# Kernel tuning notes

Hardware: AMD Instinct MI355X
Metric: run time of the kernel (lower is better)

The kernel has to match this reference:

```python
import jax, jax.numpy as jnp
import numpy as np

NUM_EXPERTS_TOTAL = 9  # 8 routed + 1 shared (shared expert is also routed via softmax in this module)
TOP_K = 2


def setup_inputs() -> dict:
    key = jax.random.key(0)
    k0, k1, k2, k3, k4 = jax.random.split(key, 5)
    B, S, H, I = 2, 2048, 1024, 2816
    E = NUM_EXPERTS_TOTAL
    x = jax.random.normal(k0, (B, S, H), dtype=jnp.float32)
    Wr = (jax.random.normal(k1, (H, E), dtype=jnp.float32) * 0.02)          # router (no bias)
    Wg = (jax.random.normal(k2, (E, H, I), dtype=jnp.float32) * 0.02)       # gate_proj per expert
    Wu = (jax.random.normal(k3, (E, H, I), dtype=jnp.float32) * 0.02)       # up_proj per expert
    Wd = (jax.random.normal(k4, (E, I, H), dtype=jnp.float32) * 0.02)       # down_proj per expert
    return {"x": x, "Wr": Wr, "Wg": Wg, "Wu": Wu, "Wd": Wd}


def reference(x, Wr, Wg, Wu, Wd):
    B, S, H = x.shape
    E = NUM_EXPERTS_TOTAL
    T = B * S

    # Router: softmax over all 9 experts, then top-2 and renormalize
    logits = jnp.einsum('bsh,he->bse', x, Wr)
    probs = jax.nn.softmax(logits, axis=-1)
    topk_w, topk_idx = jax.lax.top_k(probs, TOP_K)                 # [B,S,K]
    topk_w = topk_w / jnp.sum(topk_w, axis=-1, keepdims=True)

    xf = x.reshape(T, H)
    wf = topk_w.reshape(T, TOP_K)
    idxf = topk_idx.reshape(T, TOP_K)

    # Per-token combine weight for each expert (0 if not selected)
    cw = jnp.zeros((T, E), dtype=x.dtype).at[jnp.arange(T)[:, None], idxf].add(wf)  # [T,E]

    # SwiGLU MLP for every expert (tokens with cw==0 contribute nothing)
    gate = jax.nn.silu(jnp.einsum('th,ehi->tei', xf, Wg))          # [T,E,I]
    hidden = gate * jnp.einsum('th,ehi->tei', xf, Wu)              # [T,E,I]
    out = jnp.einsum('tei,eih,te->th', hidden, Wd, cw)             # weighted combine
    return out.reshape(B, S, H)
```

## Files before the change

### kernel.cpp

```cpp
#include <hip/hip_runtime.h>
#include <cstdint>
#include <cstddef>

#define T_TOK 4096
#define H_DIM 1024
#define I_DIM 2816
#define E_NUM 9
#define MAXTILE 76

typedef __bf16 bf16;
typedef bf16 bf16x4 __attribute__((ext_vector_type(4)));
typedef bf16 bf16x8 __attribute__((ext_vector_type(8)));
typedef float f32x4 __attribute__((ext_vector_type(4)));

constexpr int BM = 128, BN = 128, BK = 32;
constexpr int HTILE = BM * BK;
constexpr size_t HI = (size_t)H_DIM * I_DIM;

constexpr int XCAST_BLKS  = T_TOK * H_DIM / 2048;
constexpr int TGU_BLKS    = (I_DIM / 64) * (H_DIM / 64) * 2 * E_NUM;
constexpr int ROUTER_BLKS = T_TOK / 4;
constexpr int PRE1_BLKS   = XCAST_BLKS + TGU_BLKS + ROUTER_BLKS;

constexpr int GU_BLKS = (I_DIM / BN) * MAXTILE;
constexpr int TD_BLKS = (H_DIM / 64) * (I_DIM / 64) * E_NUM;
constexpr int MAIN1_BLKS = GU_BLKS + TD_BLKS;

#define GL16(gp, lp)                                                                   \
  __builtin_amdgcn_global_load_lds((const __attribute__((address_space(1))) void*)(gp), \
                                   (__attribute__((address_space(3))) void*)(lp), 16, 0, 0)

__device__ __forceinline__ void transpose_tile(float* __restrict__ tile,
                                               const float* __restrict__ src,
                                               bf16* __restrict__ dst, int R, int C,
                                               int bx, int by) {
  int r0 = by * 64, c0 = bx * 64;
  int t = threadIdx.x;
#pragma unroll
  for (int h = 0; h < 4; ++h) {
    int idx = h * 256 + t;
    int row = idx >> 4;
    int col = (idx & 15) * 4;
    GL16(src + (size_t)(r0 + row) * C + c0 + col, &tile[idx * 4]);
  }
  __syncthreads();
  int oc = t >> 2;
  int q  = t & 3;
  bf16x8 w0, w1;
#pragma unroll
  for (int j = 0; j < 8; ++j) w0[j] = (bf16)tile[(q * 16 + j) * 64 + oc];
#pragma unroll
  for (int j = 0; j < 8; ++j) w1[j] = (bf16)tile[(q * 16 + 8 + j) * 64 + oc];
  bf16* dp = dst + (size_t)(c0 + oc) * R + r0 + q * 16;
  *reinterpret_cast<bf16x8*>(dp)     = w0;
  *reinterpret_cast<bf16x8*>(dp + 8) = w1;
}

__global__ __launch_bounds__(256) void k_pre1(const float* __restrict__ x,
                                              bf16* __restrict__ xb,
                                              const float* __restrict__ Wg,
                                              const float* __restrict__ Wu,
                                              bf16* __restrict__ WgT,
                                              bf16* __restrict__ WuT,
                                              const float* __restrict__ Wr,
                                              int* __restrict__ ridx,
                                              float* __restrict__ rw,
                                              int* __restrict__ counts) {
  __shared__ float tile[64 * 64];
  int b = blockIdx.x;

  if (b < XCAST_BLKS) {
    size_t i = ((size_t)b * 256 + threadIdx.x) * 8;
    float4 a = *reinterpret_cast<const float4*>(x + i);
    float4 c = *reinterpret_cast<const float4*>(x + i + 4);
    bf16x8 v;
    v[0]=(bf16)a.x; v[1]=(bf16)a.y; v[2]=(bf16)a.z; v[3]=(bf16)a.w;
    v[4]=(bf16)c.x; v[5]=(bf16)c.y; v[6]=(bf16)c.z; v[7]=(bf16)c.w;
    *reinterpret_cast<bf16x8*>(xb + i) = v;
    return;
  }
  b -= XCAST_BLKS;

  if (b < TGU_BLKS) {
    int bx = b % (I_DIM / 64);
    int rest = b / (I_DIM / 64);
    int by = rest % (H_DIM / 64);
    int z  = rest / (H_DIM / 64);
    const float* src = (z < 9) ? (Wg + (size_t)z * HI) : (Wu + (size_t)(z - 9) * HI);
    bf16* dst = (z < 9) ? (WgT + (size_t)z * HI) : (WuT + (size_t)(z - 9) * HI);
    transpose_tile(tile, src, dst, H_DIM, I_DIM, bx, by);
    return;
  }
  b -= TGU_BLKS;

  {
    int lane = threadIdx.x & 63;
    int wid  = threadIdx.x >> 6;
    int t = b * 4 + wid;
    const float* xr = x + (size_t)t * H_DIM;
    float acc[E_NUM];
#pragma unroll
    for (int e = 0; e < E_NUM; ++e) acc[e] = 0.f;
    for (int h = lane; h < H_DIM; h += 64) {
      float xv = xr[h];
      const float* wr = Wr + h * E_NUM;
#pragma unroll
      for (int e = 0; e < E_NUM; ++e) acc[e] += xv * wr[e];
    }
#pragma unroll
    for (int off = 32; off > 0; off >>= 1) {
#pragma unroll
      for (int e = 0; e < E_NUM; ++e) acc[e] += __shfl_xor(acc[e], off);
    }
    if (lane == 0) {
      int i0 = 0;
#pragma unroll
      for (int e = 1; e < E_NUM; ++e) if (acc[e] > acc[i0]) i0 = e;
      int i1 = (i0 == 0) ? 1 : 0;
#pragma unroll
      for (int e = 0; e < E_NUM; ++e) if (e != i0 && acc[e] > acc[i1]) i1 = e;
      float r  = expf(acc[i1] - acc[i0]);
      float w0 = 1.f / (1.f + r);
      float w1 = r / (1.f + r);
      ridx[2 * t]     = i0;
      ridx[2 * t + 1] = i1;
      rw[2 * t]     = w0;
      rw[2 * t + 1] = w1;
      atomicAdd(&counts[i0], 1);
      atomicAdd(&counts[i1], 1);
    }
  }
}

__global__ void k_scan(const int* __restrict__ counts, int* __restrict__ offsets,
                       int* __restrict__ cursor, int* __restrict__ tiles,
                       int* __restrict__ n_tiles) {
  if (threadIdx.x == 0) {
    int s = 0, nt = 0;
    for (int e = 0; e < E_NUM; ++e) {
      offsets[e] = s;
      int c = counts[e];
      for (int pt = 0; pt * BM < c && nt < MAXTILE; ++pt) tiles[nt++] = (e << 16) | pt;
      s += c;
    }
    offsets[E_NUM] = s;
    *n_tiles = nt;
  }
  if (threadIdx.x < E_NUM) cursor[threadIdx.x] = 0;
}

__global__ __launch_bounds__(256) void k_scatter(const int* __restrict__ ridx,
                                                 const int* __restrict__ offsets,
                                                 int* __restrict__ cursor,
                                                 int* __restrict__ perm) {
  int t = blockIdx.x * 256 + threadIdx.x;
  if (t >= T_TOK) return;
#pragma unroll
  for (int k = 0; k < 2; ++k) {
    int e = ridx[2 * t + k];
    int pos = atomicAdd(&cursor[e], 1);
    perm[offsets[e] + pos] = 2 * t + k;
  }
}

__global__ __launch_bounds__(256, 2) void k_main1(const bf16* __restrict__ xb,
                                                  const bf16* __restrict__ WgT,
                                                  const bf16* __restrict__ WuT,
                                                  const int* __restrict__ perm,
                                                  const int* __restrict__ offsets,
                                                  const int* __restrict__ tiles,
                                                  const int* __restrict__ n_tiles,
                                                  bf16* __restrict__ hidden,
                                                  const float* __restrict__ Wd,
                                                  bf16* __restrict__ WdT) {
  __shared__ char smem[6 * HTILE * 2];
  int b = blockIdx.x;

  if (b >= GU_BLKS) {
    b -= GU_BLKS;
    int bx = b % (H_DIM / 64);
    int rest = b / (H_DIM / 64);
    int by = rest % (I_DIM / 64);
    int z  = rest / (I_DIM / 64);
    transpose_tile((float*)smem, Wd + (size_t)z * HI, WdT + (size_t)z * HI,
                   I_DIM, H_DIM, bx, by);
    return;
  }

  int ty = b / (I_DIM / BN);
  int n0 = (b % (I_DIM / BN)) * BN;
  if (ty >= *n_tiles) return;
  int tv = tiles[ty];
  int e = tv >> 16, pt = tv & 0xffff;
  int seg0 = offsets[e], cnt = offsets[e + 1] - seg0;

  bf16* As = (bf16*)smem;
  bf16* Bg = As + 2 * HTILE;
  bf16* Bu = As + 4 * HTILE;

  int tid = threadIdx.x, lane = tid & 63, wid = tid >> 6;
  int wm = wid >> 1, wn = wid & 1, l15 = lane & 15, l16 = lane >> 4;

  int srow1 = tid >> 2, srow2 = 64 + srow1;
  int kc = (tid & 3) * 8;
  int p1 = pt * BM + srow1, p2 = pt * BM + srow2;
  const bf16* a1 = xb + (size_t)(perm[seg0 + (p1 < cnt ? p1 : 0)] >> 1) * H_DIM + kc;
  const bf16* a2 = xb + (size_t)(perm[seg0 + (p2 < cnt ? p2 : 0)] >> 1) * H_DIM + kc;
  const bf16* g1 = WgT + ((size_t)e * I_DIM + n0 + srow1) * H_DIM + kc;
  const bf16* g2 = WgT + ((size_t)e * I_DIM + n0 + srow2) * H_DIM + kc;
  const bf16* u1 = WuT + ((size_t)e * I_DIM + n0 + srow1) * H_DIM + kc;
  const bf16* u2 = WuT + ((size_t)e * I_DIM + n0 + srow2) * H_DIM + kc;
  bf16* lA1 = &As[tid * 8];       bf16* lA2 = &As[2048 + tid * 8];
  bf16* lG1 = &Bg[tid * 8];       bf16* lG2 = &Bg[2048 + tid * 8];
  bf16* lU1 = &Bu[tid * 8];       bf16* lU2 = &Bu[2048 + tid * 8];

  f32x4 accg[4][4], accu[4][4];
#pragma unroll
  for (int m = 0; m < 4; ++m)
#pragma unroll
    for (int n = 0; n < 4; ++n) {
      accg[m][n] = (f32x4){0.f, 0.f, 0.f, 0.f};
      accu[m][n] = (f32x4){0.f, 0.f, 0.f, 0.f};
    }

  for (int k0 = 0; k0 < H_DIM; k0 += 2 * BK) {
    GL16(a1 + k0, lA1);            GL16(a2 + k0, lA2);
    GL16(a1 + k0 + BK, lA1 + HTILE); GL16(a2 + k0 + BK, lA2 + HTILE);
    GL16(g1 + k0, lG1);            GL16(g2 + k0, lG2);
    GL16(g1 + k0 + BK, lG1 + HTILE); GL16(g2 + k0 + BK, lG2 + HTILE);
    GL16(u1 + k0, lU1);            GL16(u2 + k0, lU2);
    GL16(u1 + k0 + BK, lU1 + HTILE); GL16(u2 + k0 + BK, lU2 + HTILE);
    __syncthreads();

#pragma unroll
    for (int kk = 0; kk < 2; ++kk) {
      const bf16* Ab = &As[kk * HTILE];
      const bf16* Gb = &Bg[kk * HTILE];
      const bf16* Ub = &Bu[kk * HTILE];
      bf16x8 af[4], bg[4], bu[4];
#pragma unroll
      for (int m = 0; m < 4; ++m)
        af[m] = *reinterpret_cast<const bf16x8*>(&Ab[(wm * 64 + m * 16 + l15) * BK + l16 * 8]);
#pragma unroll
      for (int n = 0; n < 4; ++n) {
        bg[n] = *reinterpret_cast<const bf16x8*>(&Gb[(wn * 64 + n * 16 + l15) * BK + l16 * 8]);
        bu[n] = *reinterpret_cast<const bf16x8*>(&Ub[(wn * 64 + n * 16 + l15) * BK + l16 * 8]);
      }
#pragma unroll
      for (int m = 0; m < 4; ++m)
#pragma unroll
        for (int n = 0; n < 4; ++n) {
          accg[m][n] = __builtin_amdgcn_mfma_f32_16x16x32_bf16(af[m], bg[n], accg[m][n], 0, 0, 0);
          accu[m][n] = __builtin_amdgcn_mfma_f32_16x16x32_bf16(af[m], bu[n], accu[m][n], 0, 0, 0);
        }
    }
    __syncthreads();
  }

#pragma unroll
  for (int m = 0; m < 4; ++m) {
#pragma unroll
    for (int r = 0; r < 4; ++r) {
      int p_glob = pt * BM + wm * 64 + m * 16 + l16 * 4 + r;
      if (p_glob < cnt) {
        bf16* hrow = hidden + (size_t)(seg0 + p_glob) * I_DIM;
#pragma unroll
        for (int n = 0; n < 4; ++n) {
          int col = n0 + wn * 64 + n * 16 + l15;
          float g = accg[m][n][r];
          float u = accu[m][n][r];
          float h = g / (1.f + __expf(-g)) * u;
          hrow[col] = (bf16)h;
        }
      }
    }
  }
}

__global__ __launch_bounds__(256, 2) void k_down(const bf16* __restrict__ hidden,
                                                 const bf16* __restrict__ WdT,
                                                 const int* __restrict__ perm,
                                                 const int* __restrict__ offsets,
                                                 const int* __restrict__ tiles,
                                                 const int* __restrict__ n_tiles,
                                                 bf16* __restrict__ pair_half) {
  if ((int)blockIdx.y >= *n_tiles) return;
  int tv = tiles[blockIdx.y];
  int e = tv >> 16, pt = tv & 0xffff;
  int seg0 = offsets[e], cnt = offsets[e + 1] - seg0;
  int n0 = blockIdx.x * BN;
  int kz = blockIdx.z * (I_DIM / 2);
  bf16* pout = pair_half + (size_t)blockIdx.z * 2 * T_TOK * H_DIM;

  __shared__ bf16 As[2 * HTILE];
  __shared__ bf16 Bs[2 * HTILE];

  int tid = threadIdx.x, lane = tid & 63, wid = tid >> 6;
  int wm = wid >> 1, wn = wid & 1, l15 = lane & 15, l16 = lane >> 4;

  int srow1 = tid >> 2, srow2 = 64 + srow1;
  int kc = (tid & 3) * 8;
  int p1 = pt * BM + srow1, p2 = pt * BM + srow2;
  const bf16* a1 = hidden + (size_t)(seg0 + (p1 < cnt ? p1 : 0)) * I_DIM + kz + kc;
  const bf16* a2 = hidden + (size_t)(seg0 + (p2 < cnt ? p2 : 0)) * I_DIM + kz + kc;
  const bf16* b1 = WdT + ((size_t)e * H_DIM + n0 + srow1) * I_DIM + kz + kc;
  const bf16* b2 = WdT + ((size_t)e * H_DIM + n0 + srow2) * I_DIM + kz + kc;
  bf16* lA1 = &As[tid * 8];  bf16* lA2 = &As[2048 + tid * 8];
  bf16* lB1 = &Bs[tid * 8];  bf16* lB2 = &Bs[2048 + tid * 8];

  f32x4 acc[4][4];
#pragma unroll
  for (int m = 0; m < 4; ++m)
#pragma unroll
    for (int n = 0; n < 4; ++n) acc[m][n] = (f32x4){0.f, 0.f, 0.f, 0.f};

  for (int k0 = 0; k0 < I_DIM / 2; k0 += 2 * BK) {
    GL16(a1 + k0, lA1);            GL16(a2 + k0, lA2);
    GL16(a1 + k0 + BK, lA1 + HTILE); GL16(a2 + k0 + BK, lA2 + HTILE);
    GL16(b1 + k0, lB1);            GL16(b2 + k0, lB2);
    GL16(b1 + k0 + BK, lB1 + HTILE); GL16(b2 + k0 + BK, lB2 + HTILE);
    __syncthreads();

#pragma unroll
    for (int kk = 0; kk < 2; ++kk) {
      const bf16* Ab = &As[kk * HTILE];
      const bf16* Bb = &Bs[kk * HTILE];
      bf16x8 af[4], bfr[4];
#pragma unroll
      for (int m = 0; m < 4; ++m)
        af[m] = *reinterpret_cast<const bf16x8*>(&Ab[(wm * 64 + m * 16 + l15) * BK + l16 * 8]);
#pragma unroll
      for (int n = 0; n < 4; ++n)
        bfr[n] = *reinterpret_cast<const bf16x8*>(&Bb[(wn * 64 + n * 16 + l15) * BK + l16 * 8]);
#pragma unroll
      for (int m = 0; m < 4; ++m)
#pragma unroll
        for (int n = 0; n < 4; ++n)
          acc[m][n] = __builtin_amdgcn_mfma_f32_16x16x32_bf16(af[m], bfr[n], acc[m][n], 0, 0, 0);
    }
    __syncthreads();
  }

#pragma unroll
  for (int m = 0; m < 4; ++m) {
#pragma unroll
    for (int r = 0; r < 4; ++r) {
      int p_glob = pt * BM + wm * 64 + m * 16 + l16 * 4 + r;
      if (p_glob < cnt) {
        int pair = perm[seg0 + p_glob];
        bf16* orow = pout + (size_t)pair * H_DIM;
#pragma unroll
        for (int n = 0; n < 4; ++n) {
          int col = n0 + wn * 64 + n * 16 + l15;
          orow[col] = (bf16)acc[m][n][r];
        }
      }
    }
  }
}

__global__ __launch_bounds__(256) void k_combine(const bf16* __restrict__ pair_half,
                                                 const float* __restrict__ rw,
                                                 float* __restrict__ out) {
  int t = blockIdx.x;
  int c = threadIdx.x;
  const bf16* z0 = pair_half;
  const bf16* z1 = pair_half + (size_t)2 * T_TOK * H_DIM;
  float w0 = rw[2 * t];
  float w1 = rw[2 * t + 1];
  size_t r0 = (size_t)(2 * t) * H_DIM + c * 4;
  size_t r1 = (size_t)(2 * t + 1) * H_DIM + c * 4;
  bf16x4 a0 = *reinterpret_cast<const bf16x4*>(z0 + r0);
  bf16x4 a1 = *reinterpret_cast<const bf16x4*>(z1 + r0);
  bf16x4 b0 = *reinterpret_cast<const bf16x4*>(z0 + r1);
  bf16x4 b1 = *reinterpret_cast<const bf16x4*>(z1 + r1);
  float4 o;
  o.x = w0 * ((float)a0[0] + (float)a1[0]) + w1 * ((float)b0[0] + (float)b1[0]);
  o.y = w0 * ((float)a0[1] + (float)a1[1]) + w1 * ((float)b0[1] + (float)b1[1]);
  o.z = w0 * ((float)a0[2] + (float)a1[2]) + w1 * ((float)b0[2] + (float)b1[2]);
  o.w = w0 * ((float)a0[3] + (float)a1[3]) + w1 * ((float)b0[3] + (float)b1[3]);
  *reinterpret_cast<float4*>(out + (size_t)t * H_DIM + c * 4) = o;
}

extern "C" void kernel_launch(void* const* d_in, const int* in_sizes, int n_in,
                              void* d_out, int out_size, void* d_ws, size_t ws_size,
                              hipStream_t stream) {
  const float* x  = (const float*)d_in[0];
  const float* Wr = (const float*)d_in[1];
  const float* Wg = (const float*)d_in[2];
  const float* Wu = (const float*)d_in[3];
  const float* Wd = (const float*)d_in[4];
  float* out = (float*)d_out;

  char* ws = (char*)d_ws;
  int*   counts  = (int*)(ws);
  int*   cursor  = (int*)(ws + 256);
  int*   offsets = (int*)(ws + 512);
  int*   n_tiles = (int*)(ws + 768);
  int*   tiles   = (int*)(ws + 1024);
  int*   ridx    = (int*)(ws + 64 * 1024);
  float* rw      = (float*)(ws + 128 * 1024);
  int*   perm    = (int*)(ws + 192 * 1024);
  bf16*  xb      = (bf16*)(ws + (1ull << 20));
  bf16*  WgT     = (bf16*)(ws + (16ull << 20));
  bf16*  WuT     = (bf16*)(ws + (66ull << 20));
  bf16*  WdT     = (bf16*)(ws + (116ull << 20));
  bf16*  hidden  = (bf16*)(ws + (166ull << 20));
  bf16*  pair_half = (bf16*)(ws + (212ull << 20));

  hipMemsetAsync(counts, 0, 64, stream);
  k_pre1<<<dim3(PRE1_BLKS), dim3(256), 0, stream>>>(
      x, xb, Wg, Wu, WgT, WuT, Wr, ridx, rw, counts);
  k_scan<<<dim3(1), dim3(64), 0, stream>>>(counts, offsets, cursor, tiles, n_tiles);
  k_scatter<<<dim3((T_TOK + 255) / 256), dim3(256), 0, stream>>>(ridx, offsets, cursor, perm);
  k_main1<<<dim3(MAIN1_BLKS), dim3(256), 0, stream>>>(
      xb, WgT, WuT, perm, offsets, tiles, n_tiles, hidden, Wd, WdT);
  k_down<<<dim3(H_DIM / BN, MAXTILE, 2), dim3(256), 0, stream>>>(
      hidden, WdT, perm, offsets, tiles, n_tiles, pair_half);
  k_combine<<<dim3(T_TOK), dim3(256), 0, stream>>>(pair_half, rw, out);
}
```

Baseline: 441.4 us.

## Fuse gate/up weight transpose-cast into grouped GEMM B-tile loads

Removes the separate pre-pass that transposed and cast the fp32 gate and up weights to bf16. The grouped gate/up GEMM now reads fp32 weights directly, converts them in registers and writes them into padded LDS rows (stride 40) in the K-major layout the MFMA loads expect. This drops a full read-write pass over the Wg/Wu weights. In exchange, each expert's weights are re-read in fp32 by every token tile, doubling the bytes per load, and the async global-to-LDS loads for B become synchronous strided scalar loads.

Measured after the change: 671.5 us. +52.2%, slower.

```diff
diff --git a/kernel.cpp b/kernel.cpp
--- a/kernel.cpp
+++ b/kernel.cpp
@@ -15,12 +15,13 @@
 
 constexpr int BM = 128, BN = 128, BK = 32;
 constexpr int HTILE = BM * BK;
+constexpr int BROW  = 40;
+constexpr int BH    = BN * BROW;
 constexpr size_t HI = (size_t)H_DIM * I_DIM;
 
 constexpr int XCAST_BLKS  = T_TOK * H_DIM / 2048;
-constexpr int TGU_BLKS    = (I_DIM / 64) * (H_DIM / 64) * 2 * E_NUM;
 constexpr int ROUTER_BLKS = T_TOK / 4;
-constexpr int PRE1_BLKS   = XCAST_BLKS + TGU_BLKS + ROUTER_BLKS;
+constexpr int PRE1_BLKS   = XCAST_BLKS + ROUTER_BLKS;
 
 constexpr int GU_BLKS = (I_DIM / BN) * MAXTILE;
 constexpr int TD_BLKS = (H_DIM / 64) * (I_DIM / 64) * E_NUM;
@@ -33,9 +34,8 @@
 __device__ __forceinline__ void transpose_tile(float* __restrict__ tile,
                                                const float* __restrict__ src,
                                                bf16* __restrict__ dst, int R, int C,
-                                               int bx, int by) {
+                                               int bx, int by, int t) {
   int r0 = by * 64, c0 = bx * 64;
-  int t = threadIdx.x;
 #pragma unroll
   for (int h = 0; h < 4; ++h) {
     int idx = h * 256 + t;
@@ -58,17 +58,11 @@
 
 __global__ __launch_bounds__(256) void k_pre1(const float* __restrict__ x,
                                               bf16* __restrict__ xb,
-                                              const float* __restrict__ Wg,
-                                              const float* __restrict__ Wu,
-                                              bf16* __restrict__ WgT,
-                                              bf16* __restrict__ WuT,
                                               const float* __restrict__ Wr,
                                               int* __restrict__ ridx,
                                               float* __restrict__ rw,
                                               int* __restrict__ counts) {
-  __shared__ float tile[64 * 64];
   int b = blockIdx.x;
-
   if (b < XCAST_BLKS) {
     size_t i = ((size_t)b * 256 + threadIdx.x) * 8;
     float4 a = *reinterpret_cast<const float4*>(x + i);
@@ -80,19 +74,6 @@
     return;
   }
   b -= XCAST_BLKS;
-
-  if (b < TGU_BLKS) {
-    int bx = b % (I_DIM / 64);
-    int rest = b / (I_DIM / 64);
-    int by = rest % (H_DIM / 64);
-    int z  = rest / (H_DIM / 64);
-    const float* src = (z < 9) ? (Wg + (size_t)z * HI) : (Wu + (size_t)(z - 9) * HI);
-    bf16* dst = (z < 9) ? (WgT + (size_t)z * HI) : (WuT + (size_t)(z - 9) * HI);
-    transpose_tile(tile, src, dst, H_DIM, I_DIM, bx, by);
-    return;
-  }
-  b -= TGU_BLKS;
-
   {
     int lane = threadIdx.x & 63;
     int wid  = threadIdx.x >> 6;
@@ -164,8 +145,8 @@
 }
 
 __global__ __launch_bounds__(256, 2) void k_main1(const bf16* __restrict__ xb,
-                                                  const bf16* __restrict__ WgT,
-                                                  const bf16* __restrict__ WuT,
+                                                  const float* __restrict__ Wg,
+                                                  const float* __restrict__ Wu,
                                                   const int* __restrict__ perm,
                                                   const int* __restrict__ offsets,
                                                   const int* __restrict__ tiles,
@@ -173,7 +154,7 @@
                                                   bf16* __restrict__ hidden,
                                                   const float* __restrict__ Wd,
                                                   bf16* __restrict__ WdT) {
-  __shared__ char smem[6 * HTILE * 2];
+  __shared__ char smem[2 * HTILE * 2 + 4 * BH * 2];
   int b = blockIdx.x;
 
   if (b >= GU_BLKS) {
@@ -183,7 +164,7 @@
     int by = rest % (I_DIM / 64);
     int z  = rest / (I_DIM / 64);
     transpose_tile((float*)smem, Wd + (size_t)z * HI, WdT + (size_t)z * HI,
-                   I_DIM, H_DIM, bx, by);
+                   I_DIM, H_DIM, bx, by, threadIdx.x);
     return;
   }
 
@@ -196,7 +177,7 @@
 
   bf16* As = (bf16*)smem;
   bf16* Bg = As + 2 * HTILE;
-  bf16* Bu = As + 4 * HTILE;
+  bf16* Bu = Bg + 2 * BH;
 
   int tid = threadIdx.x, lane = tid & 63, wid = tid >> 6;
   int wm = wid >> 1, wn = wid & 1, l15 = lane & 15, l16 = lane >> 4;
@@ -206,13 +187,10 @@
   int p1 = pt * BM + srow1, p2 = pt * BM + srow2;
   const bf16* a1 = xb + (size_t)(perm[seg0 + (p1 < cnt ? p1 : 0)] >> 1) * H_DIM + kc;
   const bf16* a2 = xb + (size_t)(perm[seg0 + (p2 < cnt ? p2 : 0)] >> 1) * H_DIM + kc;
-  const bf16* g1 = WgT + ((size_t)e * I_DIM + n0 + srow1) * H_DIM + kc;
-  const bf16* g2 = WgT + ((size_t)e * I_DIM + n0 + srow2) * H_DIM + kc;
-  const bf16* u1 = WuT + ((size_t)e * I_DIM + n0 + srow1) * H_DIM + kc;
-  const bf16* u2 = WuT + ((size_t)e * I_DIM + n0 + srow2) * H_DIM + kc;
   bf16* lA1 = &As[tid * 8];       bf16* lA2 = &As[2048 + tid * 8];
-  bf16* lG1 = &Bg[tid * 8];       bf16* lG2 = &Bg[2048 + tid * 8];
-  bf16* lU1 = &Bu[tid * 8];       bf16* lU2 = &Bu[2048 + tid * 8];
+
+  const float* gsrc = Wg + (size_t)e * HI + n0;
+  const float* usrc = Wu + (size_t)e * HI + n0;
 
   f32x4 accg[4][4], accu[4][4];
 #pragma unroll
@@ -224,27 +202,43 @@
     }
 
   for (int k0 = 0; k0 < H_DIM; k0 += 2 * BK) {
-    GL16(a1 + k0, lA1);            GL16(a2 + k0, lA2);
+    GL16(a1 + k0, lA1);              GL16(a2 + k0, lA2);
     GL16(a1 + k0 + BK, lA1 + HTILE); GL16(a2 + k0 + BK, lA2 + HTILE);
-    GL16(g1 + k0, lG1);            GL16(g2 + k0, lG2);
-    GL16(g1 + k0 + BK, lG1 + HTILE); GL16(g2 + k0 + BK, lG2 + HTILE);
-    GL16(u1 + k0, lU1);            GL16(u2 + k0, lU2);
-    GL16(u1 + k0 + BK, lU1 + HTILE); GL16(u2 + k0 + BK, lU2 + HTILE);
+#pragma unroll
+    for (int s = 0; s < 2; ++s) {
+      int kbase = k0 + s * BK;
+#pragma unroll
+      for (int rep = 0; rep < 4; ++rep) {
+        int q  = rep * 256 + tid;
+        int n  = q & 127;
+        int kq = q >> 7;
+        const float* gp = gsrc + (size_t)(kbase + kq * 4) * I_DIM + n;
+        const float* up = usrc + (size_t)(kbase + kq * 4) * I_DIM + n;
+        bf16x4 wg, wu;
+#pragma unroll
+        for (int j = 0; j < 4; ++j) {
+          wg[j] = (bf16)gp[(size_t)j * I_DIM];
+          wu[j] = (bf16)up[(size_t)j * I_DIM];
+        }
+        *reinterpret_cast<bf16x4*>(&Bg[s * BH + n * BROW + kq * 4]) = wg;
+        *reinterpret_cast<bf16x4*>(&Bu[s * BH + n * BROW + kq * 4]) = wu;
+      }
+    }
     __syncthreads();
 
 #pragma unroll
     for (int kk = 0; kk < 2; ++kk) {
       const bf16* Ab = &As[kk * HTILE];
-      const bf16* Gb = &Bg[kk * HTILE];
-      const bf16* Ub = &Bu[kk * HTILE];
+      const bf16* Gb = &Bg[kk * BH];
+      const bf16* Ub = &Bu[kk * BH];
       bf16x8 af[4], bg[4], bu[4];
 #pragma unroll
       for (int m = 0; m < 4; ++m)
         af[m] = *reinterpret_cast<const bf16x8*>(&Ab[(wm * 64 + m * 16 + l15) * BK + l16 * 8]);
 #pragma unroll
       for (int n = 0; n < 4; ++n) {
-        bg[n] = *reinterpret_cast<const bf16x8*>(&Gb[(wn * 64 + n * 16 + l15) * BK + l16 * 8]);
-        bu[n] = *reinterpret_cast<const bf16x8*>(&Ub[(wn * 64 + n * 16 + l15) * BK + l16 * 8]);
+        bg[n] = *reinterpret_cast<const bf16x8*>(&Gb[(wn * 64 + n * 16 + l15) * BROW + l16 * 8]);
+        bu[n] = *reinterpret_cast<const bf16x8*>(&Ub[(wn * 64 + n * 16 + l15) * BROW + l16 * 8]);
       }
 #pragma unroll
       for (int m = 0; m < 4; ++m)
@@ -402,19 +396,16 @@
   float* rw      = (float*)(ws + 128 * 1024);
   int*   perm    = (int*)(ws + 192 * 1024);
   bf16*  xb      = (bf16*)(ws + (1ull << 20));
-  bf16*  WgT     = (bf16*)(ws + (16ull << 20));
-  bf16*  WuT     = (bf16*)(ws + (66ull << 20));
   bf16*  WdT     = (bf16*)(ws + (116ull << 20));
   bf16*  hidden  = (bf16*)(ws + (166ull << 20));
   bf16*  pair_half = (bf16*)(ws + (212ull << 20));
 
   hipMemsetAsync(counts, 0, 64, stream);
-  k_pre1<<<dim3(PRE1_BLKS), dim3(256), 0, stream>>>(
-      x, xb, Wg, Wu, WgT, WuT, Wr, ridx, rw, counts);
+  k_pre1<<<dim3(PRE1_BLKS), dim3(256), 0, stream>>>(x, xb, Wr, ridx, rw, counts);
   k_scan<<<dim3(1), dim3(64), 0, stream>>>(counts, offsets, cursor, tiles, n_tiles);
   k_scatter<<<dim3((T_TOK + 255) / 256), dim3(256), 0, stream>>>(ridx, offsets, cursor, perm);
   k_main1<<<dim3(MAIN1_BLKS), dim3(256), 0, stream>>>(
-      xb, WgT, WuT, perm, offsets, tiles, n_tiles, hidden, Wd, WdT);
+      xb, Wg, Wu, perm, offsets, tiles, n_tiles, hidden, Wd, WdT);
   k_down<<<dim3(H_DIM / BN, MAXTILE, 2), dim3(256), 0, stream>>>(
       hidden, WdT, perm, offsets, tiles, n_tiles, pair_half);
   k_combine<<<dim3(T_TOK), dim3(256), 0, stream>>>(pair_half, rw, out);
```
